# Kernel optimization log

Hardware: AMD Instinct MI355X
Metric: run time of the kernel (lower is better)

## Reference

```python
import jax, jax.numpy as jnp
import numpy as np

B, T, DK, DV, N = 4, 1024, 128, 128, 65536
TOPK = 32

def setup_inputs() -> dict:
    key = jax.random.key(0)
    k1, k2, k3 = jax.random.split(key, 3)
    q = jax.random.normal(k1, (B, T, DK), dtype=jnp.float32)
    keys = jax.random.normal(k2, (N, DK), dtype=jnp.float32)
    values = jax.random.normal(k3, (N, DV), dtype=jnp.float32)
    return {"q": q, "keys": keys, "values": values, "topk": TOPK}

def reference(q, keys, values, topk):
    # scores: [B, T, N] dense dot-product score matrix
    scores = jnp.einsum('btd,nd->btn', q, keys)
    k = min(topk, keys.shape[0])
    _, idx = jax.lax.top_k(scores, k)          # idx: [B, T, k]
    K_mem = keys[idx]                          # [B, T, k, Dk] gather
    V_mem = values[idx]                        # [B, T, k, Dv] gather
    return (K_mem, V_mem)
```

## Files before the change

### kernel.cpp

```cpp
#include <hip/hip_runtime.h>
#include <float.h>

#define NQ      4096
#define NKEYS   65536
#define DKDIM   128
#define DVDIM   128
#define TOPK_N  32
#define NSPLIT  16
#define KPS     (NKEYS / NSPLIT)
#define BQ      128
#define NCAND   (NSPLIT * TOPK_N)
#define NARROW  128
#define NOUT    ((size_t)NQ * TOPK_N * DKDIM)
#define KPT     64
#define NT      (KPS / KPT)

typedef __attribute__((ext_vector_type(8))) short short8;
typedef __attribute__((ext_vector_type(4))) float v4f;

__device__ inline unsigned short f2bf(float f) {
    unsigned int u = __float_as_uint(f);
    return (unsigned short)((u + 0x7FFFu + ((u >> 16) & 1u)) >> 16);
}

__device__ inline unsigned packpk(float s, unsigned li) {
    unsigned u = __float_as_uint(s);
    u = ((int)u < 0) ? ~u : (u | 0x80000000u);
    return (u & 0xFFFFF000u) | (4095u - li);
}
__device__ inline float unpack_lb(unsigned pk) {
    const unsigned m = pk & 0xFFFFF000u;
    const unsigned b = (m & 0x80000000u) ? (m & 0x7FFFFFFFu) : ~m;
    return __uint_as_float(b);
}

#define CEXU(p, s, desc) {                                                  \
    const unsigned _o = (unsigned)__shfl_xor((int)(p), (s));                \
    const bool _first = (p) > _o;                                           \
    const bool _keep  = (_first == (((l16 & (s)) == 0) == (desc)));         \
    (p) = _keep ? (p) : _o; }
#define CEXUI(pa, pb) { if ((pb) > (pa)) { const unsigned _t=(pa); (pa)=(pb); (pb)=_t; } }

__device__ __forceinline__ void sortmergeU(
    unsigned& p0, unsigned& p1, const int cc,
    const unsigned* __restrict__ bqr, const int l16)
{
    unsigned s0 = (l16      < cc) ? bqr[l16]      : 0u;
    unsigned s1 = (l16 + 16 < cc) ? bqr[l16 + 16] : 0u;

    CEXU(s0, 1, ((l16 & 2) == 0)); CEXU(s1, 1, ((l16 & 2) == 0));
    CEXU(s0, 2, ((l16 & 4) == 0)); CEXU(s1, 2, ((l16 & 4) == 0));
    CEXU(s0, 1, ((l16 & 4) == 0)); CEXU(s1, 1, ((l16 & 4) == 0));
    CEXU(s0, 4, ((l16 & 8) == 0)); CEXU(s1, 4, ((l16 & 8) == 0));
    CEXU(s0, 2, ((l16 & 8) == 0)); CEXU(s1, 2, ((l16 & 8) == 0));
    CEXU(s0, 1, ((l16 & 8) == 0)); CEXU(s1, 1, ((l16 & 8) == 0));
    CEXU(s0, 8, true);  CEXU(s1, 8, false);
    CEXU(s0, 4, true);  CEXU(s1, 4, false);
    CEXU(s0, 2, true);  CEXU(s1, 2, false);
    CEXU(s0, 1, true);  CEXU(s1, 1, false);
    CEXUI(s0, s1);
    CEXU(s0, 8, true);  CEXU(s1, 8, true);
    CEXU(s0, 4, true);  CEXU(s1, 4, true);
    CEXU(s0, 2, true);  CEXU(s1, 2, true);
    CEXU(s0, 1, true);  CEXU(s1, 1, true);

    unsigned c0 = (unsigned)__shfl_xor((int)s1, 15);
    unsigned c1 = (unsigned)__shfl_xor((int)s0, 15);

    CEXUI(p0, c0);
    CEXUI(p1, c1);
    CEXUI(p0, p1);
    CEXU(p0, 8, true); CEXU(p1, 8, true);
    CEXU(p0, 4, true); CEXU(p1, 4, true);
    CEXU(p0, 2, true); CEXU(p1, 2, true);
    CEXU(p0, 1, true); CEXU(p1, 1, true);
}

__global__ __launch_bounds__(256) void convert_kernel(
    const float* __restrict__ q, const float* __restrict__ keys,
    unsigned short* __restrict__ qbf, unsigned short* __restrict__ kbf)
{
    const size_t QG = (size_t)NQ * DKDIM / 8;
    const size_t KG = (size_t)NKEYS * DKDIM / 8;
    const size_t g  = (size_t)blockIdx.x * 256 + threadIdx.x;
    if (g >= QG + KG) return;
    const float* src;
    unsigned short* dst;
    if (g < QG) { src = q + g * 8;         dst = qbf + g * 8; }
    else        { const size_t h = g - QG; src = keys + h * 8; dst = kbf + h * 8; }
    const float4 a = ((const float4*)src)[0];
    const float4 b = ((const float4*)src)[1];
    short8 o;
    o[0] = (short)f2bf(a.x); o[1] = (short)f2bf(a.y);
    o[2] = (short)f2bf(a.z); o[3] = (short)f2bf(a.w);
    o[4] = (short)f2bf(b.x); o[5] = (short)f2bf(b.y);
    o[6] = (short)f2bf(b.z); o[7] = (short)f2bf(b.w);
    *(short8*)dst = o;
}

__global__ __launch_bounds__(512, 4) void score_select_kernel(
    const unsigned short* __restrict__ qbf, const unsigned short* __restrict__ kbf,
    unsigned* __restrict__ cand)
{
    __shared__ unsigned short kst[2][KPT * DKDIM];
    __shared__ unsigned bq[BQ][33];

    const int tid  = threadIdx.x;
    const int wave = tid >> 6;
    const int lane = tid & 63;
    const int l16  = lane & 15;
    const int quad = lane >> 4;

    const int lin   = blockIdx.y * gridDim.x + blockIdx.x;
    const int split = ((lin & 7) << 1) | (lin >> 8);
    const int qgrp  = (lin >> 3) & 31;
    const int q0    = qgrp * BQ + wave * 16;
    const int nbase = split * KPS;

    unsigned* __restrict__ bqr = &bq[wave * 16 + l16][0];

    short8 afrag[4];
#pragma unroll
    for (int t = 0; t < 4; ++t)
        afrag[t] = *(const short8*)(qbf + (size_t)(q0 + l16) * DKDIM + t * 32 + quad * 8);

    unsigned pk0[4], pk1[4];
#pragma unroll
    for (int r = 0; r < 4; ++r) { pk0[r] = 0u; pk1[r] = 0u; }
    float vmf = -FLT_MAX;
    int   cnt = 0;

    auto select32 = [&](const v4f a1, const v4f a2, const int n0loc) {
        const int h0 = a1[0] > vmf, h1 = a1[1] > vmf, h2 = a1[2] > vmf, h3 = a1[3] > vmf;
        const int h4 = a2[0] > vmf, h5 = a2[1] > vmf, h6 = a2[2] > vmf, h7 = a2[3] > vmf;
        const int nh = h0 + h1 + h2 + h3 + h4 + h5 + h6 + h7;
        const int s16   = __shfl_xor(nh, 16);
        const int psum  = nh + s16;
        const int sx32  = __shfl_xor(psum, 32);
        const int nhcol = psum + sx32;
        if (__ballot(cnt + nhcol > 32)) {
#pragma unroll
            for (int r = 0; r < 4; ++r) {
                const int cc = __shfl(cnt, quad * 4 + r);
                sortmergeU(pk0[r], pk1[r], cc, &bq[wave * 16 + quad * 4 + r][0], l16);
            }
            const unsigned t0 = (unsigned)__shfl((int)pk1[0], (l16 >> 2) * 16 + 15);
            const unsigned t1 = (unsigned)__shfl((int)pk1[1], (l16 >> 2) * 16 + 15);
            const unsigned t2 = (unsigned)__shfl((int)pk1[2], (l16 >> 2) * 16 + 15);
            const unsigned t3 = (unsigned)__shfl((int)pk1[3], (l16 >> 2) * 16 + 15);
            const unsigned a01 = (l16 & 1) ? t1 : t0;
            const unsigned a23 = (l16 & 1) ? t3 : t2;
            vmf = unpack_lb((l16 & 2) ? a23 : a01);
            cnt = 0;
        }
        int pos = cnt + ((quad & 1) ? s16 : 0) + ((quad & 2) ? sx32 : 0);
        const unsigned lb = (unsigned)(n0loc + quad * 4);
        if (h0) { bqr[pos] = packpk(a1[0], lb);      ++pos; }
        if (h1) { bqr[pos] = packpk(a1[1], lb + 1);  ++pos; }
        if (h2) { bqr[pos] = packpk(a1[2], lb + 2);  ++pos; }
        if (h3) { bqr[pos] = packpk(a1[3], lb + 3);  ++pos; }
        if (h4) { bqr[pos] = packpk(a2[0], lb + 16); ++pos; }
        if (h5) { bqr[pos] = packpk(a2[1], lb + 17); ++pos; }
        if (h6) { bqr[pos] = packpk(a2[2], lb + 18); ++pos; }
        if (h7) { bqr[pos] = packpk(a2[3], lb + 19); }
        cnt += nhcol;
    };

    const unsigned short* ksrc = kbf + (size_t)nbase * DKDIM;
    const int c0 = tid, c1 = tid + 512;
    const int d0 = ((c0 >> 4) * 128) + (((c0 & 15) ^ ((c0 >> 4) & 7)) * 8);
    const int d1 = ((c1 >> 4) * 128) + (((c1 & 15) ^ ((c1 >> 4) & 7)) * 8);
    const int sx = l16 & 7;

    {
        const short8 a = *(const short8*)(ksrc + c0 * 8);
        const short8 b = *(const short8*)(ksrc + c1 * 8);
        *(short8*)&kst[0][d0] = a;
        *(short8*)&kst[0][d1] = b;
    }
    __syncthreads();

    int cur = 0;
    for (int t = 0; t < NT; ++t) {
        short8 nA, nB;
        const bool more = (t + 1 < NT);
        if (more) {
            const unsigned short* s = ksrc + (size_t)(t + 1) * (KPT * DKDIM);
            nA = *(const short8*)(s + c0 * 8);
            nB = *(const short8*)(s + c1 * 8);
        }
#pragma unroll
        for (int half = 0; half < 2; ++half) {
            const unsigned short* kr0 = &kst[cur][(half * 32 + l16) * 128];
            const unsigned short* kr1 = &kst[cur][(half * 32 + 16 + l16) * 128];
            v4f acc1 = {0.f, 0.f, 0.f, 0.f};
            v4f acc2 = {0.f, 0.f, 0.f, 0.f};
#pragma unroll
            for (int tt = 0; tt < 4; ++tt) {
                const short8 b0 = *(const short8*)(kr0 + ((quad + tt * 4) ^ sx) * 8);
                const short8 b1 = *(const short8*)(kr1 + ((quad + tt * 4) ^ sx) * 8);
                acc1 = __builtin_amdgcn_mfma_f32_16x16x32_bf16(b0, afrag[tt], acc1, 0, 0, 0);
                acc2 = __builtin_amdgcn_mfma_f32_16x16x32_bf16(b1, afrag[tt], acc2, 0, 0, 0);
            }
            select32(acc1, acc2, t * KPT + half * 32);
        }
        if (more) {
            *(short8*)&kst[cur ^ 1][d0] = nA;
            *(short8*)&kst[cur ^ 1][d1] = nB;
        }
        __syncthreads();
        cur ^= 1;
    }

#pragma unroll
    for (int r = 0; r < 4; ++r) {
        const int cc = __shfl(cnt, quad * 4 + r);
        sortmergeU(pk0[r], pk1[r], cc, &bq[wave * 16 + quad * 4 + r][0], l16);
        const size_t base = ((size_t)(q0 + quad * 4 + r) * NSPLIT + split) * TOPK_N;
        cand[base + l16]      = pk0[r];
        cand[base + 16 + l16] = pk1[r];
    }
}

__global__ __launch_bounds__(512) void rescore_gather_kernel(
    const float* __restrict__ qg, const float* __restrict__ keys,
    const float* __restrict__ values, const unsigned* __restrict__ cand,
    float* __restrict__ out)
{
    __shared__ float    qrow[DKDIM];
    __shared__ unsigned spk[NCAND];
    __shared__ int      spn[NCAND];
    __shared__ float    ssv[NARROW];
    __shared__ int      ssi[NARROW];
    const int bt  = blockIdx.x;
    const int tid = threadIdx.x;

    if (tid < DKDIM) qrow[tid] = qg[(size_t)bt * DKDIM + tid];

    unsigned pk = cand[(size_t)bt * NCAND + tid];
    int      n  = (tid >> 5) * KPS + (int)(4095u - (pk & 0xFFFu));

    for (int k = 2; k <= NCAND; k <<= 1) {
        for (int j = k >> 1; j > 0; j >>= 1) {
            unsigned opk; int on;
            if (j >= 64) {
                __syncthreads();
                spk[tid] = pk; spn[tid] = n;
                __syncthreads();
                opk = spk[tid ^ j]; on = spn[tid ^ j];
            } else {
                opk = (unsigned)__shfl_xor((int)pk, j);
                on  = __shfl_xor(n, j);
            }
            const bool dir  = ((tid & k) == 0);
            const bool mineFirst = (pk > opk) || (pk == opk && n < on);
            const bool keep = (((tid & j) == 0) == (mineFirst == dir));
            if (!keep) { pk = opk; n = on; }
        }
    }
    __syncthreads();

    float sc = -FLT_MAX;
    if (tid < NARROW) {
        const float4* krow = (const float4*)(keys + (size_t)n * DKDIM);
        float s = 0.f;
#pragma unroll
        for (int d4 = 0; d4 < DKDIM / 4; ++d4) {
            const float4 k4 = krow[d4];
            const float4 q4 = *(const float4*)&qrow[4 * d4];
            s = fmaf(q4.x, k4.x, s);
            s = fmaf(q4.y, k4.y, s);
            s = fmaf(q4.z, k4.z, s);
            s = fmaf(q4.w, k4.w, s);
        }
        sc = s;
    } else {
        n = 0x7FFFFFFF;
    }

    for (int k = 2; k <= NARROW; k <<= 1) {
        for (int j = k >> 1; j > 0; j >>= 1) {
            float of; int on;
            if (j >= 64) {
                __syncthreads();
                if (tid < NARROW) { ssv[tid] = sc; ssi[tid] = n; }
                __syncthreads();
                const int p = (tid ^ j) & (NARROW - 1);
                of = ssv[p]; on = ssi[p];
            } else {
                of = __shfl_xor(sc, j);
                on = __shfl_xor(n, j);
            }
            const bool dir  = ((tid & k) == 0);
            const bool mineFirst = (sc > of) || (sc == of && n < on);
            const bool keep = (((tid & j) == 0) == (mineFirst == dir));
            if (!keep) { sc = of; n = on; }
        }
    }

    __syncthreads();
    if (tid < TOPK_N) ssi[tid] = n;
    __syncthreads();

    const int lane = tid & 31;
    const int rb   = tid >> 5;
#pragma unroll
    for (int r = 0; r < 2; ++r) {
        const int row = rb + 16 * r;
        const int nn  = ssi[row];
        const float4 kv = *(const float4*)(keys   + (size_t)nn * DKDIM + 4 * lane);
        const float4 vv = *(const float4*)(values + (size_t)nn * DVDIM + 4 * lane);
        const size_t ob = ((size_t)bt * TOPK_N + row) * DKDIM + 4 * lane;
        *(float4*)(out + ob)        = kv;
        *(float4*)(out + NOUT + ob) = vv;
    }
}

extern "C" void kernel_launch(void* const* d_in, const int* in_sizes, int n_in,
                              void* d_out, int out_size, void* d_ws, size_t ws_size,
                              hipStream_t stream)
{
    const float* q      = (const float*)d_in[0];
    const float* keys   = (const float*)d_in[1];
    const float* values = (const float*)d_in[2];
    float* out = (float*)d_out;

    unsigned short* qbf = (unsigned short*)d_ws;
    unsigned short* kbf = (unsigned short*)((char*)d_ws + (1u << 20));
    unsigned* cand = (unsigned*)((char*)d_ws + (17u << 20));

    const int cvt_groups = (NQ + NKEYS) * DKDIM / 8;
    convert_kernel<<<(cvt_groups + 255) / 256, 256, 0, stream>>>(q, keys, qbf, kbf);
    score_select_kernel<<<dim3(NQ / BQ, NSPLIT), 512, 0, stream>>>(qbf, kbf, cand);
    rescore_gather_kernel<<<NQ, 512, 0, stream>>>(q, keys, values, cand, out);
}
```

Baseline: 555.3 us.

## Double key splits to 32 and narrow exact rescoring to 64 candidates

The score/select kernel now splits the key set into 32 chunks instead of 16. This doubles the block count and halves each block's key range, giving more parallelism and shorter serial select loops. The rescore kernel must now bitonic-sort 1024 packed candidates (two per thread), which adds shared-memory sort stages and syncs. In exchange, it rescoring only the top 64 in fp32 and sorts them in a single wave using shuffles only. Narrowing to 64 raises the risk that a bf16 ranking error drops a true top-32 key.

```diff
diff --git a/kernel.cpp b/kernel.cpp
--- a/kernel.cpp
+++ b/kernel.cpp
@@ -6,11 +6,11 @@
 #define DKDIM   128
 #define DVDIM   128
 #define TOPK_N  32
-#define NSPLIT  16
+#define NSPLIT  32
 #define KPS     (NKEYS / NSPLIT)
 #define BQ      128
 #define NCAND   (NSPLIT * TOPK_N)
-#define NARROW  128
+#define NARROW  64
 #define NOUT    ((size_t)NQ * TOPK_N * DKDIM)
 #define KPT     64
 #define NT      (KPS / KPT)
@@ -112,8 +112,9 @@
     const int quad = lane >> 4;
 
     const int lin   = blockIdx.y * gridDim.x + blockIdx.x;
-    const int split = ((lin & 7) << 1) | (lin >> 8);
-    const int qgrp  = (lin >> 3) & 31;
+    const int rest  = lin >> 3;
+    const int split = ((lin & 7) << 2) | (rest & 3);
+    const int qgrp  = rest >> 2;
     const int q0    = qgrp * BQ + wave * 16;
     const int nbase = split * KPS;
 
@@ -230,37 +231,52 @@
     __shared__ float    qrow[DKDIM];
     __shared__ unsigned spk[NCAND];
     __shared__ int      spn[NCAND];
-    __shared__ float    ssv[NARROW];
-    __shared__ int      ssi[NARROW];
+    __shared__ int      ssi[TOPK_N];
     const int bt  = blockIdx.x;
     const int tid = threadIdx.x;
 
     if (tid < DKDIM) qrow[tid] = qg[(size_t)bt * DKDIM + tid];
 
-    unsigned pk = cand[(size_t)bt * NCAND + tid];
-    int      n  = (tid >> 5) * KPS + (int)(4095u - (pk & 0xFFFu));
+    unsigned pkA = cand[(size_t)bt * NCAND + tid];
+    unsigned pkB = cand[(size_t)bt * NCAND + tid + 512];
+    int nA = (tid >> 5) * KPS + (int)(4095u - (pkA & 0xFFFu));
+    int nB = ((tid + 512) >> 5) * KPS + (int)(4095u - (pkB & 0xFFFu));
 
     for (int k = 2; k <= NCAND; k <<= 1) {
         for (int j = k >> 1; j > 0; j >>= 1) {
-            unsigned opk; int on;
+            if (j == 512) {
+                const bool bFirst = (pkB > pkA) || (pkB == pkA && nB < nA);
+                if (bFirst) {
+                    const unsigned tp = pkA; pkA = pkB; pkB = tp;
+                    const int      tn = nA;  nA  = nB;  nB  = tn;
+                }
+                continue;
+            }
+            unsigned oA, oB; int mA, mB;
             if (j >= 64) {
                 __syncthreads();
-                spk[tid] = pk; spn[tid] = n;
+                spk[tid] = pkA; spn[tid] = nA;
+                spk[tid + 512] = pkB; spn[tid + 512] = nB;
                 __syncthreads();
-                opk = spk[tid ^ j]; on = spn[tid ^ j];
+                oA = spk[tid ^ j];           mA = spn[tid ^ j];
+                oB = spk[(tid ^ j) + 512];   mB = spn[(tid ^ j) + 512];
             } else {
-                opk = (unsigned)__shfl_xor((int)pk, j);
-                on  = __shfl_xor(n, j);
-            }
-            const bool dir  = ((tid & k) == 0);
-            const bool mineFirst = (pk > opk) || (pk == opk && n < on);
-            const bool keep = (((tid & j) == 0) == (mineFirst == dir));
-            if (!keep) { pk = opk; n = on; }
+                oA = (unsigned)__shfl_xor((int)pkA, j); mA = __shfl_xor(nA, j);
+                oB = (unsigned)__shfl_xor((int)pkB, j); mB = __shfl_xor(nB, j);
+            }
+            const bool dirA = ((tid & k) == 0);
+            const bool dirB = (((tid + 512) & k) == 0);
+            const bool upper = ((tid & j) == 0);
+            const bool fA = (pkA > oA) || (pkA == oA && nA < mA);
+            const bool fB = (pkB > oB) || (pkB == oB && nB < mB);
+            if (!(upper == (fA == dirA))) { pkA = oA; nA = mA; }
+            if (!(upper == (fB == dirB))) { pkB = oB; nB = mB; }
         }
     }
     __syncthreads();
 
     float sc = -FLT_MAX;
+    int   n  = nA;
     if (tid < NARROW) {
         const float4* krow = (const float4*)(keys + (size_t)n * DKDIM);
         float s = 0.f;
@@ -274,32 +290,21 @@
             s = fmaf(q4.w, k4.w, s);
         }
         sc = s;
-    } else {
-        n = 0x7FFFFFFF;
-    }
-
-    for (int k = 2; k <= NARROW; k <<= 1) {
-        for (int j = k >> 1; j > 0; j >>= 1) {
-            float of; int on;
-            if (j >= 64) {
-                __syncthreads();
-                if (tid < NARROW) { ssv[tid] = sc; ssi[tid] = n; }
-                __syncthreads();
-                const int p = (tid ^ j) & (NARROW - 1);
-                of = ssv[p]; on = ssi[p];
-            } else {
-                of = __shfl_xor(sc, j);
-                on = __shfl_xor(n, j);
-            }
-            const bool dir  = ((tid & k) == 0);
-            const bool mineFirst = (sc > of) || (sc == of && n < on);
-            const bool keep = (((tid & j) == 0) == (mineFirst == dir));
-            if (!keep) { sc = of; n = on; }
-        }
-    }
-
-    __syncthreads();
-    if (tid < TOPK_N) ssi[tid] = n;
+    }
+
+    if (tid < 64) {
+        for (int k = 2; k <= NARROW; k <<= 1) {
+            for (int j = k >> 1; j > 0; j >>= 1) {
+                const float of = __shfl_xor(sc, j);
+                const int   on = __shfl_xor(n, j);
+                const bool dir  = ((tid & k) == 0);
+                const bool mineFirst = (sc > of) || (sc == of && n < on);
+                const bool keep = (((tid & j) == 0) == (mineFirst == dir));
+                if (!keep) { sc = of; n = on; }
+            }
+        }
+        if (tid < TOPK_N) ssi[tid] = n;
+    }
     __syncthreads();
 
     const int lane = tid & 31;
```

New measurement: 639.2 us. +15.1%, slower.
